# Performance work log

Measured on AMD Instinct MI355X. Metric: run time of the kernel, lower is better.

Reference implementation:

```python
import jax, jax.numpy as jnp
import numpy as np

B, S, D = 2, 2048, 1024
H, DK = 16, 64            # n_heads, d_k = d_model // n_heads
EXP = 4                   # pattern-separation expand_factor
ED = DK * EXP             # expanded_dim = 256
TOPK = 32                 # top-k kept after ReLU expansion
ALPHA = 0.05
TNT = 1.0                 # trace_norm_target


def setup_inputs() -> dict:
    key = jax.random.key(0)
    ks = jax.random.split(key, 8)
    sc = 1.0 / np.sqrt(D)
    x = jax.random.normal(ks[0], (B, S, D), jnp.float32)
    W_q = jax.random.normal(ks[1], (D, D), jnp.float32) * sc
    W_k = jax.random.normal(ks[2], (D, D), jnp.float32) * sc
    W_v = jax.random.normal(ks[3], (D, D), jnp.float32) * sc
    W_o = jax.random.normal(ks[4], (D, D), jnp.float32) * sc
    # trace buffers (non-zero so the trace read path actually matters)
    traces = jax.random.normal(ks[5], (H, DK, DK), jnp.float32) * 0.02
    value_traces = jax.random.normal(ks[6], (H, ED, DK), jnp.float32) * 0.02
    # frozen random expansion projection (dentate gyrus), W / sqrt(d_k)
    W_expand = jax.random.normal(ks[7], (DK, ED), jnp.float32) / np.sqrt(DK)
    return dict(x=x, W_q=W_q, W_k=W_k, W_v=W_v, W_o=W_o,
                traces=traces, value_traces=value_traces, W_expand=W_expand)


def _eff_alpha(T):
    # alpha / (1 + ||T_h||_F / trace_norm_target), shape (1, H, 1, 1)
    norms = jnp.sqrt(jnp.sum(T * T, axis=(1, 2)))
    return (ALPHA / (1.0 + norms / TNT)).reshape(1, -1, 1, 1)


def _forward(x, W_q, W_k, W_v, W_o, traces, value_traces, W_expand):
    b, s, d = x.shape
    def proj(W):
        return jnp.einsum('bsd,de->bse', x, W).reshape(b, s, H, DK).transpose(0, 2, 1, 3)
    Q, K, V = proj(W_q), proj(W_k), proj(W_v)  # (B, H, S, DK)

    scores = jnp.einsum('bhqd,bhkd->bhqk', Q, K)
    # score trace bias: alpha_eff * (Q @ T @ K^T)
    QT = jnp.einsum('bhqd,hde->bhqe', Q, traces)
    trace_scores = jnp.einsum('bhqe,bhke->bhqk', QT, K)
    scores = (scores + _eff_alpha(traces) * trace_scores) / np.sqrt(DK)
    A = jax.nn.softmax(scores, axis=-1)
    out = jnp.einsum('bhqk,bhkd->bhqd', A, V)

    # value trace read with use_key_q shift: address with previous token's Q
    Q_addr = jnp.concatenate([jnp.zeros_like(Q[:, :, :1, :]), Q[:, :, :-1, :]], axis=2)
    # pattern separation: frozen random expansion + ReLU + top-k sparsify
    Q_exp = jax.nn.relu(jnp.einsum('bhsd,de->bhse', Q_addr, W_expand))  # (B,H,S,ED)
    kth = jax.lax.top_k(Q_exp, TOPK)[0][..., -1:]
    Q_sparse = jnp.where(Q_exp >= kth, Q_exp, 0.0)  # == scatter of top-k vals (ties at 0 contribute 0)
    stored = jnp.einsum('bhse,hed->bhsd', Q_sparse, value_traces)
    out = out + _eff_alpha(value_traces) * stored

    out = out.transpose(0, 2, 1, 3).reshape(b, s, d)
    return jnp.einsum('bsd,de->bse', out, W_o)


def reference(x, W_q, W_k, W_v, W_o, traces, value_traces, W_expand):
    return _forward(x, W_q, W_k, W_v, W_o, traces, value_traces, W_expand)
```

## Files before the change

kernel.cpp:

```cpp
#include <hip/hip_runtime.h>
#include <stdint.h>

#define Bn 2
#define Sn 2048
#define Dn 1024
#define Hn 16
#define DKn 64
#define EDn 256

typedef __attribute__((ext_vector_type(8))) short bvec8;
typedef __attribute__((ext_vector_type(4))) float fvec4;

#define MFMA(a, b, c) __builtin_amdgcn_mfma_f32_16x16x32_bf16(a, b, c, 0, 0, 0)

__device__ __forceinline__ float b2f(unsigned short u) {
  return __uint_as_float(((unsigned)u) << 16);
}
__device__ __forceinline__ unsigned short f2b(float x) {
  unsigned u = __float_as_uint(x);
  u += 0x7fffu + ((u >> 16) & 1u);
  return (unsigned short)(u >> 16);
}
__device__ __forceinline__ void g2l(const unsigned short* g, unsigned short* l) {
  __builtin_amdgcn_global_load_lds(
      (const __attribute__((address_space(1))) void*)g,
      (__attribute__((address_space(3))) void*)l, 16, 0, 0);
}

__global__ __launch_bounds__(256) void k_alphas(
    const float* __restrict__ traces, const float* __restrict__ vtr,
    float* __restrict__ alphas) {
  int blk = blockIdx.x;
  const float* base;
  int n;
  if (blk < 16) { base = traces + blk * DKn * DKn; n = DKn * DKn; }
  else          { base = vtr + (blk - 16) * EDn * DKn; n = EDn * DKn; }
  float s = 0.f;
  for (int i = threadIdx.x; i < n; i += 256) { float v = base[i]; s += v * v; }
  __shared__ float red[256];
  red[threadIdx.x] = s;
  __syncthreads();
  for (int off = 128; off > 0; off >>= 1) {
    if (threadIdx.x < off) red[threadIdx.x] += red[threadIdx.x + off];
    __syncthreads();
  }
  if (threadIdx.x == 0) alphas[blk] = 0.05f / (1.f + sqrtf(red[0]));
}

__global__ __launch_bounds__(256) void k_trW(
    const float* __restrict__ w0, const float* __restrict__ w1,
    const float* __restrict__ w2, const float* __restrict__ w3,
    unsigned short* __restrict__ dst) {
  int z = blockIdx.z;
  const float* src = (z == 0) ? w0 : ((z == 1) ? w1 : ((z == 2) ? w2 : w3));
  unsigned short* d = dst + (size_t)z * Dn * Dn;
  __shared__ unsigned short Tl[64][72];
  int tid = threadIdx.x;
  int k0 = blockIdx.y * 64, n0 = blockIdx.x * 64;
#pragma unroll
  for (int i = 0; i < 4; ++i) {
    int q = tid + 256 * i;
    int kr = q >> 4, c4 = q & 15;
    float4 v = *(const float4*)&src[(size_t)(k0 + kr) * Dn + n0 + 4 * c4];
    ushort4 u;
    u.x = f2b(v.x); u.y = f2b(v.y); u.z = f2b(v.z); u.w = f2b(v.w);
    *(ushort4*)&Tl[kr][4 * c4] = u;
  }
  __syncthreads();
#pragma unroll
  for (int i = 0; i < 4; ++i) {
    int q = tid + 256 * i;
    int nr = q >> 4, c4 = q & 15;
    ushort4 u;
    u.x = Tl[4 * c4 + 0][nr]; u.y = Tl[4 * c4 + 1][nr];
    u.z = Tl[4 * c4 + 2][nr]; u.w = Tl[4 * c4 + 3][nr];
    *(ushort4*)&d[(size_t)(n0 + nr) * Dn + k0 + 4 * c4] = u;
  }
}

__global__ __launch_bounds__(256) void k_mkM(const float* __restrict__ tr,
                                             const float* __restrict__ alph,
                                             unsigned short* __restrict__ Mt) {
  int h = blockIdx.x;
  float a = alph[h] * 0.125f;
  const float* th = tr + (size_t)h * DKn * DKn;
  unsigned short* mh = Mt + (size_t)h * DKn * DKn;
  for (int i = threadIdx.x; i < DKn * DKn; i += 256) {
    int e = i >> 6, k = i & 63;
    float v = a * th[(size_t)k * DKn + e] + ((e == k) ? 0.125f : 0.f);
    mh[i] = f2b(v);
  }
}

__global__ __launch_bounds__(256) void k_trE(const float* __restrict__ Wexp,
                                             unsigned short* __restrict__ WexpT) {
  int e0 = blockIdx.x * 64;
  __shared__ unsigned short Tl[64][72];
  int tid = threadIdx.x;
#pragma unroll
  for (int i = 0; i < 4; ++i) {
    int q = tid + 256 * i;
    int dr = q >> 4, c4 = q & 15;
    float4 v = *(const float4*)&Wexp[(size_t)dr * EDn + e0 + 4 * c4];
    ushort4 u;
    u.x = f2b(v.x); u.y = f2b(v.y); u.z = f2b(v.z); u.w = f2b(v.w);
    *(ushort4*)&Tl[dr][4 * c4] = u;
  }
  __syncthreads();
#pragma unroll
  for (int i = 0; i < 4; ++i) {
    int q = tid + 256 * i;
    int er = q >> 4, c4 = q & 15;
    ushort4 u;
    u.x = Tl[4 * c4 + 0][er]; u.y = Tl[4 * c4 + 1][er];
    u.z = Tl[4 * c4 + 2][er]; u.w = Tl[4 * c4 + 3][er];
    *(ushort4*)&WexpT[(size_t)(e0 + er) * DKn + 4 * c4] = u;
  }
}

__global__ __launch_bounds__(256) void k_trVT(const float* __restrict__ vtr,
                                              unsigned short* __restrict__ VTt) {
  int e0 = blockIdx.x * 64;
  int h = blockIdx.y;
  const float* src = vtr + (size_t)h * EDn * DKn;
  unsigned short* dst = VTt + (size_t)h * DKn * EDn;
  __shared__ unsigned short Tl[64][72];
  int tid = threadIdx.x;
#pragma unroll
  for (int i = 0; i < 4; ++i) {
    int q = tid + 256 * i;
    int er = q >> 4, c4 = q & 15;
    float4 v = *(const float4*)&src[(size_t)(e0 + er) * DKn + 4 * c4];
    ushort4 u;
    u.x = f2b(v.x); u.y = f2b(v.y); u.z = f2b(v.z); u.w = f2b(v.w);
    *(ushort4*)&Tl[er][4 * c4] = u;
  }
  __syncthreads();
#pragma unroll
  for (int i = 0; i < 4; ++i) {
    int q = tid + 256 * i;
    int dr = q >> 4, c4 = q & 15;
    ushort4 u;
    u.x = Tl[4 * c4 + 0][dr]; u.y = Tl[4 * c4 + 1][dr];
    u.z = Tl[4 * c4 + 2][dr]; u.w = Tl[4 * c4 + 3][dr];
    *(ushort4*)&dst[(size_t)dr * EDn + e0 + 4 * c4] = u;
  }
}

__global__ __launch_bounds__(256) void k_xb(const float* __restrict__ x,
                                            unsigned short* __restrict__ xb) {
  size_t i = ((size_t)blockIdx.x * 256 + threadIdx.x) * 4;
  float4 v = *(const float4*)&x[i];
  ushort4 u;
  u.x = f2b(v.x); u.y = f2b(v.y); u.z = f2b(v.z); u.w = f2b(v.w);
  *(ushort4*)&xb[i] = u;
}

template <int MODE>
__global__ __launch_bounds__(256) void k_gemm(
    const unsigned short* __restrict__ Ab, const float* __restrict__ Af,
    const unsigned short* __restrict__ BtBase, unsigned short* __restrict__ Qb,
    unsigned short* __restrict__ Kb, unsigned short* __restrict__ VtOut,
    float* __restrict__ Cout) {
  const int z = (MODE == 0) ? blockIdx.z : 0;
  const unsigned short* Bt = BtBase + (size_t)z * Dn * Dn;
  __shared__ unsigned short As[128 * 32];
  __shared__ unsigned short Bs[128 * 32];
  const int tid = threadIdx.x;
  const int w = tid >> 6, lane = tid & 63, qd = lane >> 4, cc = lane & 15;
  const int m0 = blockIdx.y * 128, n0 = blockIdx.x * 128;
  const int mW = 64 * (w >> 1), nW = 64 * (w & 1);
  const int srow = lane >> 2;
  const int schk = 8 * ((lane & 3) ^ (srow & 3));
  const int r0 = 32 * w + srow, r1 = r0 + 16;
  fvec4 acc[4][4];
#pragma unroll
  for (int i = 0; i < 4; ++i)
#pragma unroll
    for (int j = 0; j < 4; ++j) acc[i][j] = (fvec4){0.f, 0.f, 0.f, 0.f};

  for (int k0 = 0; k0 < Dn; k0 += 32) {
    if (MODE == 0) {
      g2l(&Ab[(size_t)(m0 + r0) * Dn + k0 + schk], &As[1024 * w]);
      g2l(&Ab[(size_t)(m0 + r1) * Dn + k0 + schk], &As[1024 * w + 512]);
    } else {
#pragma unroll
      for (int i = 0; i < 4; ++i) {
        int q = tid + 256 * i;
        int row = q >> 3, c4 = q & 7;
        float4 v = *(const float4*)&Af[(size_t)(m0 + row) * Dn + k0 + 4 * c4];
        ushort4 u;
        u.x = f2b(v.x); u.y = f2b(v.y); u.z = f2b(v.z); u.w = f2b(v.w);
        *(ushort4*)&As[row * 32 + 8 * ((c4 >> 1) ^ (row & 3)) + 4 * (c4 & 1)] =
            u;
      }
    }
    g2l(&Bt[(size_t)(n0 + r0) * Dn + k0 + schk], &Bs[1024 * w]);
    g2l(&Bt[(size_t)(n0 + r1) * Dn + k0 + schk], &Bs[1024 * w + 512]);
    __syncthreads();
    bvec8 af[4], bf[4];
#pragma unroll
    for (int i = 0; i < 4; ++i) {
      int ra = mW + 16 * i + cc;
      af[i] = *(const bvec8*)&As[ra * 32 + 8 * (qd ^ (ra & 3))];
      int rb = nW + 16 * i + cc;
      bf[i] = *(const bvec8*)&Bs[rb * 32 + 8 * (qd ^ (rb & 3))];
    }
#pragma unroll
    for (int i = 0; i < 4; ++i)
#pragma unroll
      for (int j = 0; j < 4; ++j) acc[i][j] = MFMA(af[i], bf[j], acc[i][j]);
    __syncthreads();
  }
#pragma unroll
  for (int i = 0; i < 4; ++i)
#pragma unroll
    for (int j = 0; j < 4; ++j) {
      int rowb = m0 + mW + 16 * i + 4 * qd;
      int col = n0 + nW + 16 * j + cc;
      if (MODE == 0) {
        int b = rowb >> 11, s = rowb & 2047;
        int h = col >> 6, dk = col & 63;
        if (z == 2) {
          ushort4 u;
          u.x = f2b(acc[i][j][0]); u.y = f2b(acc[i][j][1]);
          u.z = f2b(acc[i][j][2]); u.w = f2b(acc[i][j][3]);
          *(ushort4*)&VtOut[(((size_t)(b * Hn + h)) * DKn + dk) * Sn + s] = u;
        } else {
          unsigned short* Cb = (z == 0) ? Qb : Kb;
#pragma unroll
          for (int r = 0; r < 4; ++r)
            Cb[(((size_t)(b * Hn + h)) * Sn + s + r) * DKn + dk] =
                f2b(acc[i][j][r]);
        }
      } else {
#pragma unroll
        for (int r = 0; r < 4; ++r)
          Cout[(size_t)(rowb + r) * Dn + col] = acc[i][j][r];
      }
    }
}

__global__ __launch_bounds__(256, 2) void k_pattsep(
    const unsigned short* __restrict__ Qb,
    const unsigned short* __restrict__ WexpT,
    const unsigned short* __restrict__ VTt,
    const float* __restrict__ alphas, float* __restrict__ AT) {
  __shared__ uint4 Wl4[2048];
  __shared__ uint4 Vl4[2048];
  __shared__ uint4 Ps4[4][256];
  const int tile = blockIdx.x, bh = blockIdx.y;
  const int b = bh >> 4, h = bh & 15;
  const int tid = threadIdx.x;
  const int w = tid >> 6, lane = tid & 63, qd = lane >> 4, cc = lane & 15;
  const float avt = alphas[16 + h];

  const uint4* wsrc = (const uint4*)WexpT;
  const uint4* vsrc = (const uint4*)(VTt + (size_t)h * DKn * EDn);
  for (int i = tid; i < 2048; i += 256) {
    int e = i >> 3, c = i & 7;
    Wl4[e * 8 + (c ^ (e & 7))] = wsrc[i];
    int d = i >> 5, c2 = i & 31;
    Vl4[d * 32 + (c2 ^ (d & 7))] = vsrc[i];
  }
  __syncthreads();

  const unsigned short* Wls = (const unsigned short*)Wl4;
  const unsigned short* Vls = (const unsigned short*)Vl4;
  unsigned short* Pw = (unsigned short*)Ps4[w];

  for (int rg = 0; rg < 2; ++rg) {
    const int s0 = tile * 128 + w * 32 + rg * 16;
    bvec8 aq0 = {}, aq1 = {};
    const int srow = s0 + cc;
    if (srow > 0) {
      const unsigned short* qp = Qb + ((size_t)bh * Sn + srow - 1) * DKn;
      aq0 = *(const bvec8*)&qp[8 * qd];
      aq1 = *(const bvec8*)&qp[32 + 8 * qd];
    }
    fvec4 E[16];
#pragma unroll
    for (int j = 0; j < 16; ++j) {
      const int e = 16 * j + cc;
      const unsigned short* wr = Wls + e * 64;
      bvec8 b0 = *(const bvec8*)&wr[8 * (qd ^ (e & 7))];
      bvec8 b1 = *(const bvec8*)&wr[8 * ((4 + qd) ^ (e & 7))];
      fvec4 zv = {0.f, 0.f, 0.f, 0.f};
      zv = MFMA(aq0, b0, zv);
      E[j] = MFMA(aq1, b1, zv);
    }
#pragma unroll
    for (int j = 0; j < 16; ++j)
#pragma unroll
      for (int r = 0; r < 4; ++r) E[j][r] = fmaxf(E[j][r], 0.f);

    float thr[4];
#pragma unroll
    for (int r = 0; r < 4; ++r) {
      unsigned cur = 0u;
      bool done = false;
      for (int bit = 30; bit >= 0; --bit) {
        unsigned cand = cur | (1u << bit);
        float t = __uint_as_float(cand);
        int cnt = 0;
#pragma unroll
        for (int j = 0; j < 16; ++j) cnt += (E[j][r] >= t) ? 1 : 0;
        cnt += __shfl_xor(cnt, 1);
        cnt += __shfl_xor(cnt, 2);
        cnt += __shfl_xor(cnt, 4);
        cnt += __shfl_xor(cnt, 8);
        if (!done && cnt >= 32) {
          cur = cand;
          if (cnt == 32) done = true;
        }
        if (__all(done)) break;
      }
      thr[r] = __uint_as_float(cur);
    }

    fvec4 acc2[4];
#pragma unroll
    for (int j2 = 0; j2 < 4; ++j2) acc2[j2] = (fvec4){0.f, 0.f, 0.f, 0.f};

#pragma unroll
    for (int half = 0; half < 2; ++half) {
#pragma unroll
      for (int j = 0; j < 8; ++j) {
        const int jj = j + 8 * half;
#pragma unroll
        for (int r = 0; r < 4; ++r) {
          float v = E[jj][r];
          bool sel = (v >= thr[r]) && (v > 0.f);
          int row = 4 * qd + r;
          int s = 16 * j + cc;
          int ch = (s >> 3) ^ (row & 7);
          Pw[row * 128 + ch * 8 + (s & 7)] = sel ? f2b(v) : (unsigned short)0;
        }
      }
#pragma unroll
      for (int j2 = 0; j2 < 4; ++j2) {
        const int d = 16 * j2 + cc;
        const unsigned short* vr = Vls + d * 256;
#pragma unroll
        for (int c = 0; c < 4; ++c) {
          int cg = 4 * (c + 4 * half) + qd;
          bvec8 bv = *(const bvec8*)&vr[8 * (cg ^ (d & 7))];
          int ca = 4 * c + qd;
          bvec8 ap = *(const bvec8*)&Pw[cc * 128 + 8 * (ca ^ (cc & 7))];
          acc2[j2] = MFMA(ap, bv, acc2[j2]);
        }
      }
    }
#pragma unroll
    for (int j2 = 0; j2 < 4; ++j2)
#pragma unroll
      for (int r = 0; r < 4; ++r) {
        int row = s0 + 4 * qd + r;
        AT[((size_t)(b * Sn + row)) * Dn + h * DKn + 16 * j2 + cc] =
            avt * acc2[j2][r];
      }
  }
}

__global__ __launch_bounds__(256) void k_attn(
    const unsigned short* __restrict__ Qb, const unsigned short* __restrict__ Kb,
    const unsigned short* __restrict__ Vt, const unsigned short* __restrict__ Mt,
    float* __restrict__ AT) {
  __shared__ unsigned short Kd[64 * 64];
  __shared__ unsigned short Vl[64 * 64];
  __shared__ unsigned short Ps[4][16][72];
  const int bh = blockIdx.x, qt = blockIdx.y;
  const int b = bh >> 4, h = bh & 15;
  const int tid = threadIdx.x;
  const int w = tid >> 6, lane = tid & 63, qd = lane >> 4, cc = lane & 15;
  const float L2E = 1.4426950408889634f;
  const float NB = 23.083120654223414f;

  const unsigned short* qg = Qb + ((size_t)bh * Sn + qt * 64 + w * 16) * DKn;
  bvec8 a0 = *(const bvec8*)&qg[cc * DKn + 8 * qd];
  bvec8 a1 = *(const bvec8*)&qg[cc * DKn + 32 + 8 * qd];
  const unsigned short* mh = Mt + (size_t)h * DKn * DKn;
#pragma unroll
  for (int j = 0; j < 4; ++j) {
    bvec8 b0 = *(const bvec8*)&mh[(size_t)(16 * j + cc) * DKn + 8 * qd];
    bvec8 b1 = *(const bvec8*)&mh[(size_t)(16 * j + cc) * DKn + 32 + 8 * qd];
    fvec4 zz = {0.f, 0.f, 0.f, 0.f};
    zz = MFMA(a0, b0, zz);
    zz = MFMA(a1, b1, zz);
#pragma unroll
    for (int r = 0; r < 4; ++r) {
      int qr = 4 * qd + r;
      Kd[(16 * w + qr) * 64 + 8 * ((2 * j + (cc >> 3)) ^ (qr & 7)) + (cc & 7)] =
          f2b(zz[r]);
    }
  }
  bvec8 aq0 = *(const bvec8*)&Kd[(16 * w + cc) * 64 + 8 * (qd ^ (cc & 7))];
  bvec8 aq1 =
      *(const bvec8*)&Kd[(16 * w + cc) * 64 + 8 * ((qd + 4) ^ (cc & 7))];

  float l_s = 0.f;
  fvec4 O[4];
#pragma unroll
  for (int j = 0; j < 4; ++j) O[j] = (fvec4){0.f, 0.f, 0.f, 0.f};

  const int vrow = lane >> 3;
  const int vchk = 8 * ((lane & 7) ^ (vrow & 7));
  const unsigned short* kgb = Kb + (size_t)bh * Sn * DKn;
  const unsigned short* vgb = Vt + (size_t)bh * DKn * Sn;

  for (int kt = 0; kt < Sn / 64; ++kt) {
    __syncthreads();
    const unsigned short* kg = kgb + (size_t)kt * 64 * DKn;
    g2l(&kg[(size_t)(16 * w + vrow) * 64 + vchk], &Kd[1024 * w]);
    g2l(&kg[(size_t)(16 * w + 8 + vrow) * 64 + vchk], &Kd[1024 * w + 512]);
    g2l(&vgb[(size_t)(16 * w + vrow) * Sn + kt * 64 + vchk], &Vl[1024 * w]);
    g2l(&vgb[(size_t)(16 * w + 8 + vrow) * Sn + kt * 64 + vchk],
        &Vl[1024 * w + 512]);
    __syncthreads();
    fvec4 sc[4];
#pragma unroll
    for (int j = 0; j < 4; ++j) {
      int rk = 16 * j + cc;
      bvec8 b0 = *(const bvec8*)&Kd[rk * 64 + 8 * (qd ^ (cc & 7))];
      bvec8 b1 = *(const bvec8*)&Kd[rk * 64 + 8 * ((qd + 4) ^ (cc & 7))];
      fvec4 zz = {0.f, 0.f, 0.f, 0.f};
      zz = MFMA(b0, aq0, zz);
      sc[j] = MFMA(b1, aq1, zz);
    }
#pragma unroll
    for (int j = 0; j < 4; ++j) {
      float p0 = __builtin_amdgcn_exp2f(fmaf(sc[j][0], L2E, -NB));
      float p1 = __builtin_amdgcn_exp2f(fmaf(sc[j][1], L2E, -NB));
      float p2 = __builtin_amdgcn_exp2f(fmaf(sc[j][2], L2E, -NB));
      float p3 = __builtin_amdgcn_exp2f(fmaf(sc[j][3], L2E, -NB));
      l_s += (p0 + p1) + (p2 + p3);
      ushort4 u;
      u.x = f2b(p0); u.y = f2b(p1); u.z = f2b(p2); u.w = f2b(p3);
      *(ushort4*)&Ps[w][cc][16 * j + 4 * qd] = u;
    }
    bvec8 ap0 = *(const bvec8*)&Ps[w][cc][8 * qd];
    bvec8 ap1 = *(const bvec8*)&Ps[w][cc][32 + 8 * qd];
#pragma unroll
    for (int j = 0; j < 4; ++j) {
      int rv = 16 * j + cc;
      bvec8 v0 = *(const bvec8*)&Vl[rv * 64 + 8 * (qd ^ (cc & 7))];
      bvec8 v1 = *(const bvec8*)&Vl[rv * 64 + 8 * ((qd + 4) ^ (cc & 7))];
      O[j] = MFMA(ap0, v0, O[j]);
      O[j] = MFMA(ap1, v1, O[j]);
    }
  }
  l_s += __shfl_xor(l_s, 16);
  l_s += __shfl_xor(l_s, 32);
  float linv = 1.f / l_s;
  float inv[4];
#pragma unroll
  for (int r = 0; r < 4; ++r) inv[r] = __shfl(linv, 4 * qd + r);
#pragma unroll
  for (int j = 0; j < 4; ++j)
#pragma unroll
    for (int r = 0; r < 4; ++r) {
      int row = qt * 64 + w * 16 + 4 * qd + r;
      float* p = AT + ((size_t)(b * Sn + row)) * Dn + h * DKn + 16 * j + cc;
      *p += O[j][r] * inv[r];
    }
}

extern "C" void kernel_launch(void* const* d_in, const int* in_sizes, int n_in,
                              void* d_out, int out_size, void* d_ws,
                              size_t ws_size, hipStream_t stream) {
  const float* x = (const float*)d_in[0];
  const float* Wq = (const float*)d_in[1];
  const float* Wk = (const float*)d_in[2];
  const float* Wv = (const float*)d_in[3];
  const float* Wo = (const float*)d_in[4];
  const float* traces = (const float*)d_in[5];
  const float* vtr = (const float*)d_in[6];
  const float* Wexp = (const float*)d_in[7];

  const size_t NQ = (size_t)Bn * Hn * Sn * DKn;
  unsigned short* Qb = (unsigned short*)d_ws;
  unsigned short* Kb = Qb + NQ;
  unsigned short* Vt = Kb + NQ;
  unsigned short* Wt = Vt + NQ;
  unsigned short* Mt = Wt + NQ;
  unsigned short* WexpT = Mt + 65536;
  unsigned short* VTt = WexpT + 16384;
  float* alph = (float*)(VTt + 262144);
  float* AT = alph + 32;
  unsigned short* xb = (unsigned short*)AT;

  k_alphas<<<32, 256, 0, stream>>>(traces, vtr, alph);
  k_trW<<<dim3(16, 16, 4), 256, 0, stream>>>(Wq, Wk, Wv, Wo, Wt);
  k_mkM<<<16, 256, 0, stream>>>(traces, alph, Mt);
  k_trE<<<4, 256, 0, stream>>>(Wexp, WexpT);
  k_trVT<<<dim3(4, 16), 256, 0, stream>>>(vtr, VTt);
  k_xb<<<4096, 256, 0, stream>>>(x, xb);
  k_gemm<0><<<dim3(8, 32, 3), 256, 0, stream>>>(xb, nullptr, Wt, Qb, Kb, Vt,
                                                nullptr);
  k_pattsep<<<dim3(16, 32), 256, 0, stream>>>(Qb, WexpT, VTt, alph, AT);
  k_attn<<<dim3(32, 32), 256, 0, stream>>>(Qb, Kb, Vt, Mt, AT);
  k_gemm<1><<<dim3(8, 32, 1), 256, 0, stream>>>(
      nullptr, AT, Wt + 3 * (size_t)Dn * Dn, nullptr, nullptr, nullptr,
      (float*)d_out);
}
```

Before: 309.5 us.

## Merge prep kernels, store attention output in bf16, transpose-free MFMA epilogues

Folds five small preprocessing kernels into one launch, which cuts launch overhead. The attention and pattern-separation output is now stored as bf16, so the final GEMM loads it with global_load_lds instead of converting fp32 per tile, and its buffer traffic is halved. The Q/K and output GEMMs swap the MFMA operands so each lane writes vectorized contiguous stores. The log2e scaling is folded into the M matrix, so softmax drops its fma and max-offset, and a cheaper bf16 pack is used for probabilities. This risks extra rounding in the accumulated output and possible overflow, since the fixed exponent offset is gone.

```diff
diff --git a/kernel.cpp b/kernel.cpp
--- a/kernel.cpp
+++ b/kernel.cpp
@@ -21,144 +21,139 @@
   u += 0x7fffu + ((u >> 16) & 1u);
   return (unsigned short)(u >> 16);
 }
+__device__ __forceinline__ unsigned pk2(float a, float b) {
+  return ((__float_as_uint(a) + 0x8000u) >> 16) |
+         ((__float_as_uint(b) + 0x8000u) & 0xffff0000u);
+}
 __device__ __forceinline__ void g2l(const unsigned short* g, unsigned short* l) {
   __builtin_amdgcn_global_load_lds(
       (const __attribute__((address_space(1))) void*)g,
       (__attribute__((address_space(3))) void*)l, 16, 0, 0);
 }
 
-__global__ __launch_bounds__(256) void k_alphas(
-    const float* __restrict__ traces, const float* __restrict__ vtr,
-    float* __restrict__ alphas) {
-  int blk = blockIdx.x;
-  const float* base;
-  int n;
-  if (blk < 16) { base = traces + blk * DKn * DKn; n = DKn * DKn; }
-  else          { base = vtr + (blk - 16) * EDn * DKn; n = EDn * DKn; }
-  float s = 0.f;
-  for (int i = threadIdx.x; i < n; i += 256) { float v = base[i]; s += v * v; }
-  __shared__ float red[256];
-  red[threadIdx.x] = s;
-  __syncthreads();
-  for (int off = 128; off > 0; off >>= 1) {
-    if (threadIdx.x < off) red[threadIdx.x] += red[threadIdx.x + off];
-    __syncthreads();
-  }
-  if (threadIdx.x == 0) alphas[blk] = 0.05f / (1.f + sqrtf(red[0]));
-}
-
-__global__ __launch_bounds__(256) void k_trW(
-    const float* __restrict__ w0, const float* __restrict__ w1,
-    const float* __restrict__ w2, const float* __restrict__ w3,
-    unsigned short* __restrict__ dst) {
-  int z = blockIdx.z;
-  const float* src = (z == 0) ? w0 : ((z == 1) ? w1 : ((z == 2) ? w2 : w3));
-  unsigned short* d = dst + (size_t)z * Dn * Dn;
+__global__ __launch_bounds__(256) void k_prep1(
+    const float* __restrict__ x, const float* __restrict__ w0,
+    const float* __restrict__ w1, const float* __restrict__ w2,
+    const float* __restrict__ w3, const float* __restrict__ traces,
+    const float* __restrict__ vtr, const float* __restrict__ Wexp,
+    unsigned short* __restrict__ Wt, unsigned short* __restrict__ WexpT,
+    unsigned short* __restrict__ xb, float* __restrict__ alphas,
+    unsigned short* __restrict__ VTt) {
+  const int blk = blockIdx.x;
+  const int tid = threadIdx.x;
   __shared__ unsigned short Tl[64][72];
-  int tid = threadIdx.x;
-  int k0 = blockIdx.y * 64, n0 = blockIdx.x * 64;
-#pragma unroll
-  for (int i = 0; i < 4; ++i) {
-    int q = tid + 256 * i;
-    int kr = q >> 4, c4 = q & 15;
-    float4 v = *(const float4*)&src[(size_t)(k0 + kr) * Dn + n0 + 4 * c4];
+  if (blk < 1024) {
+    int z = blk >> 8, t = blk & 255;
+    int n0 = (t & 15) * 64, k0 = (t >> 4) * 64;
+    const float* src = (z == 0) ? w0 : ((z == 1) ? w1 : ((z == 2) ? w2 : w3));
+    unsigned short* d = Wt + (size_t)z * Dn * Dn;
+#pragma unroll
+    for (int i = 0; i < 4; ++i) {
+      int q = tid + 256 * i;
+      int kr = q >> 4, c4 = q & 15;
+      float4 v = *(const float4*)&src[(size_t)(k0 + kr) * Dn + n0 + 4 * c4];
+      ushort4 u;
+      u.x = f2b(v.x); u.y = f2b(v.y); u.z = f2b(v.z); u.w = f2b(v.w);
+      *(ushort4*)&Tl[kr][4 * c4] = u;
+    }
+    __syncthreads();
+#pragma unroll
+    for (int i = 0; i < 4; ++i) {
+      int q = tid + 256 * i;
+      int nr = q >> 4, c4 = q & 15;
+      ushort4 u;
+      u.x = Tl[4 * c4 + 0][nr]; u.y = Tl[4 * c4 + 1][nr];
+      u.z = Tl[4 * c4 + 2][nr]; u.w = Tl[4 * c4 + 3][nr];
+      *(ushort4*)&d[(size_t)(n0 + nr) * Dn + k0 + 4 * c4] = u;
+    }
+  } else if (blk < 1028) {
+    int e0 = (blk - 1024) * 64;
+#pragma unroll
+    for (int i = 0; i < 4; ++i) {
+      int q = tid + 256 * i;
+      int dr = q >> 4, c4 = q & 15;
+      float4 v = *(const float4*)&Wexp[(size_t)dr * EDn + e0 + 4 * c4];
+      ushort4 u;
+      u.x = f2b(v.x); u.y = f2b(v.y); u.z = f2b(v.z); u.w = f2b(v.w);
+      *(ushort4*)&Tl[dr][4 * c4] = u;
+    }
+    __syncthreads();
+#pragma unroll
+    for (int i = 0; i < 4; ++i) {
+      int q = tid + 256 * i;
+      int er = q >> 4, c4 = q & 15;
+      ushort4 u;
+      u.x = Tl[4 * c4 + 0][er]; u.y = Tl[4 * c4 + 1][er];
+      u.z = Tl[4 * c4 + 2][er]; u.w = Tl[4 * c4 + 3][er];
+      *(ushort4*)&WexpT[(size_t)(e0 + er) * DKn + 4 * c4] = u;
+    }
+  } else if (blk < 5124) {
+    size_t i = ((size_t)(blk - 1028) * 256 + tid) * 4;
+    float4 v = *(const float4*)&x[i];
     ushort4 u;
     u.x = f2b(v.x); u.y = f2b(v.y); u.z = f2b(v.z); u.w = f2b(v.w);
-    *(ushort4*)&Tl[kr][4 * c4] = u;
-  }
-  __syncthreads();
-#pragma unroll
-  for (int i = 0; i < 4; ++i) {
-    int q = tid + 256 * i;
-    int nr = q >> 4, c4 = q & 15;
-    ushort4 u;
-    u.x = Tl[4 * c4 + 0][nr]; u.y = Tl[4 * c4 + 1][nr];
-    u.z = Tl[4 * c4 + 2][nr]; u.w = Tl[4 * c4 + 3][nr];
-    *(ushort4*)&d[(size_t)(n0 + nr) * Dn + k0 + 4 * c4] = u;
+    *(ushort4*)&xb[i] = u;
+  } else if (blk < 5156) {
+    int a = blk - 5124;
+    const float* base;
+    int n;
+    if (a < 16) { base = traces + a * DKn * DKn; n = DKn * DKn; }
+    else        { base = vtr + (a - 16) * EDn * DKn; n = EDn * DKn; }
+    float s = 0.f;
+    for (int i = tid; i < n; i += 256) { float v = base[i]; s += v * v; }
+    __shared__ float red[256];
+    red[tid] = s;
+    __syncthreads();
+    for (int off = 128; off > 0; off >>= 1) {
+      if (tid < off) red[tid] += red[tid + off];
+      __syncthreads();
+    }
+    if (tid == 0) alphas[a] = 0.05f / (1.f + sqrtf(red[0]));
+  } else {
+    int t = blk - 5156;
+    int e0 = (t & 3) * 64, h = t >> 2;
+    const float* src = vtr + (size_t)h * EDn * DKn;
+    unsigned short* dst = VTt + (size_t)h * DKn * EDn;
+#pragma unroll
+    for (int i = 0; i < 4; ++i) {
+      int q = tid + 256 * i;
+      int er = q >> 4, c4 = q & 15;
+      float4 v = *(const float4*)&src[(size_t)(e0 + er) * DKn + 4 * c4];
+      ushort4 u;
+      u.x = f2b(v.x); u.y = f2b(v.y); u.z = f2b(v.z); u.w = f2b(v.w);
+      *(ushort4*)&Tl[er][4 * c4] = u;
+    }
+    __syncthreads();
+#pragma unroll
+    for (int i = 0; i < 4; ++i) {
+      int q = tid + 256 * i;
+      int dr = q >> 4, c4 = q & 15;
+      ushort4 u;
+      u.x = Tl[4 * c4 + 0][dr]; u.y = Tl[4 * c4 + 1][dr];
+      u.z = Tl[4 * c4 + 2][dr]; u.w = Tl[4 * c4 + 3][dr];
+      *(ushort4*)&dst[(size_t)dr * EDn + e0 + 4 * c4] = u;
+    }
   }
 }
 
 __global__ __launch_bounds__(256) void k_mkM(const float* __restrict__ tr,
                                              const float* __restrict__ alph,
                                              unsigned short* __restrict__ Mt) {
+  const float SC = 0.125f * 1.4426950408889634f;
   int h = blockIdx.x;
-  float a = alph[h] * 0.125f;
+  float a = alph[h] * SC;
   const float* th = tr + (size_t)h * DKn * DKn;
   unsigned short* mh = Mt + (size_t)h * DKn * DKn;
   for (int i = threadIdx.x; i < DKn * DKn; i += 256) {
     int e = i >> 6, k = i & 63;
-    float v = a * th[(size_t)k * DKn + e] + ((e == k) ? 0.125f : 0.f);
+    float v = a * th[(size_t)k * DKn + e] + ((e == k) ? SC : 0.f);
     mh[i] = f2b(v);
   }
-}
-
-__global__ __launch_bounds__(256) void k_trE(const float* __restrict__ Wexp,
-                                             unsigned short* __restrict__ WexpT) {
-  int e0 = blockIdx.x * 64;
-  __shared__ unsigned short Tl[64][72];
-  int tid = threadIdx.x;
-#pragma unroll
-  for (int i = 0; i < 4; ++i) {
-    int q = tid + 256 * i;
-    int dr = q >> 4, c4 = q & 15;
-    float4 v = *(const float4*)&Wexp[(size_t)dr * EDn + e0 + 4 * c4];
-    ushort4 u;
-    u.x = f2b(v.x); u.y = f2b(v.y); u.z = f2b(v.z); u.w = f2b(v.w);
-    *(ushort4*)&Tl[dr][4 * c4] = u;
-  }
-  __syncthreads();
-#pragma unroll
-  for (int i = 0; i < 4; ++i) {
-    int q = tid + 256 * i;
-    int er = q >> 4, c4 = q & 15;
-    ushort4 u;
-    u.x = Tl[4 * c4 + 0][er]; u.y = Tl[4 * c4 + 1][er];
-    u.z = Tl[4 * c4 + 2][er]; u.w = Tl[4 * c4 + 3][er];
-    *(ushort4*)&WexpT[(size_t)(e0 + er) * DKn + 4 * c4] = u;
-  }
-}
-
-__global__ __launch_bounds__(256) void k_trVT(const float* __restrict__ vtr,
-                                              unsigned short* __restrict__ VTt) {
-  int e0 = blockIdx.x * 64;
-  int h = blockIdx.y;
-  const float* src = vtr + (size_t)h * EDn * DKn;
-  unsigned short* dst = VTt + (size_t)h * DKn * EDn;
-  __shared__ unsigned short Tl[64][72];
-  int tid = threadIdx.x;
-#pragma unroll
-  for (int i = 0; i < 4; ++i) {
-    int q = tid + 256 * i;
-    int er = q >> 4, c4 = q & 15;
-    float4 v = *(const float4*)&src[(size_t)(e0 + er) * DKn + 4 * c4];
-    ushort4 u;
-    u.x = f2b(v.x); u.y = f2b(v.y); u.z = f2b(v.z); u.w = f2b(v.w);
-    *(ushort4*)&Tl[er][4 * c4] = u;
-  }
-  __syncthreads();
-#pragma unroll
-  for (int i = 0; i < 4; ++i) {
-    int q = tid + 256 * i;
-    int dr = q >> 4, c4 = q & 15;
-    ushort4 u;
-    u.x = Tl[4 * c4 + 0][dr]; u.y = Tl[4 * c4 + 1][dr];
-    u.z = Tl[4 * c4 + 2][dr]; u.w = Tl[4 * c4 + 3][dr];
-    *(ushort4*)&dst[(size_t)dr * EDn + e0 + 4 * c4] = u;
-  }
-}
-
-__global__ __launch_bounds__(256) void k_xb(const float* __restrict__ x,
-                                            unsigned short* __restrict__ xb) {
-  size_t i = ((size_t)blockIdx.x * 256 + threadIdx.x) * 4;
-  float4 v = *(const float4*)&x[i];
-  ushort4 u;
-  u.x = f2b(v.x); u.y = f2b(v.y); u.z = f2b(v.z); u.w = f2b(v.w);
-  *(ushort4*)&xb[i] = u;
 }
 
 template <int MODE>
 __global__ __launch_bounds__(256) void k_gemm(
-    const unsigned short* __restrict__ Ab, const float* __restrict__ Af,
+    const unsigned short* __restrict__ Ab,
     const unsigned short* __restrict__ BtBase, unsigned short* __restrict__ Qb,
     unsigned short* __restrict__ Kb, unsigned short* __restrict__ VtOut,
     float* __restrict__ Cout) {
@@ -173,6 +168,7 @@
   const int srow = lane >> 2;
   const int schk = 8 * ((lane & 3) ^ (srow & 3));
   const int r0 = 32 * w + srow, r1 = r0 + 16;
+  const bool swap = (MODE == 1) || (z != 2);
   fvec4 acc[4][4];
 #pragma unroll
   for (int i = 0; i < 4; ++i)
@@ -180,21 +176,8 @@
     for (int j = 0; j < 4; ++j) acc[i][j] = (fvec4){0.f, 0.f, 0.f, 0.f};
 
   for (int k0 = 0; k0 < Dn; k0 += 32) {
-    if (MODE == 0) {
-      g2l(&Ab[(size_t)(m0 + r0) * Dn + k0 + schk], &As[1024 * w]);
-      g2l(&Ab[(size_t)(m0 + r1) * Dn + k0 + schk], &As[1024 * w + 512]);
-    } else {
-#pragma unroll
-      for (int i = 0; i < 4; ++i) {
-        int q = tid + 256 * i;
-        int row = q >> 3, c4 = q & 7;
-        float4 v = *(const float4*)&Af[(size_t)(m0 + row) * Dn + k0 + 4 * c4];
-        ushort4 u;
-        u.x = f2b(v.x); u.y = f2b(v.y); u.z = f2b(v.z); u.w = f2b(v.w);
-        *(ushort4*)&As[row * 32 + 8 * ((c4 >> 1) ^ (row & 3)) + 4 * (c4 & 1)] =
-            u;
-      }
-    }
+    g2l(&Ab[(size_t)(m0 + r0) * Dn + k0 + schk], &As[1024 * w]);
+    g2l(&Ab[(size_t)(m0 + r1) * Dn + k0 + schk], &As[1024 * w + 512]);
     g2l(&Bt[(size_t)(n0 + r0) * Dn + k0 + schk], &Bs[1024 * w]);
     g2l(&Bt[(size_t)(n0 + r1) * Dn + k0 + schk], &Bs[1024 * w + 512]);
     __syncthreads();
@@ -206,37 +189,49 @@
       int rb = nW + 16 * i + cc;
       bf[i] = *(const bvec8*)&Bs[rb * 32 + 8 * (qd ^ (rb & 3))];
     }
-#pragma unroll
-    for (int i = 0; i < 4; ++i)
-#pragma unroll
-      for (int j = 0; j < 4; ++j) acc[i][j] = MFMA(af[i], bf[j], acc[i][j]);
+    if (swap) {
+#pragma unroll
+      for (int i = 0; i < 4; ++i)
+#pragma unroll
+        for (int j = 0; j < 4; ++j) acc[i][j] = MFMA(bf[j], af[i], acc[i][j]);
+    } else {
+#pragma unroll
+      for (int i = 0; i < 4; ++i)
+#pragma unroll
+        for (int j = 0; j < 4; ++j) acc[i][j] = MFMA(af[i], bf[j], acc[i][j]);
+    }
     __syncthreads();
   }
 #pragma unroll
   for (int i = 0; i < 4; ++i)
 #pragma unroll
     for (int j = 0; j < 4; ++j) {
-      int rowb = m0 + mW + 16 * i + 4 * qd;
-      int col = n0 + nW + 16 * j + cc;
-      if (MODE == 0) {
+      if (MODE == 1) {
+        int s = m0 + mW + 16 * i + cc;
+        int nb = n0 + nW + 16 * j + 4 * qd;
+        float4 v = make_float4(acc[i][j][0], acc[i][j][1], acc[i][j][2],
+                               acc[i][j][3]);
+        *(float4*)&Cout[(size_t)s * Dn + nb] = v;
+      } else if (z == 2) {
+        int rowb = m0 + mW + 16 * i + 4 * qd;
+        int col = n0 + nW + 16 * j + cc;
         int b = rowb >> 11, s = rowb & 2047;
         int h = col >> 6, dk = col & 63;
-        if (z == 2) {
-          ushort4 u;
-          u.x = f2b(acc[i][j][0]); u.y = f2b(acc[i][j][1]);
-          u.z = f2b(acc[i][j][2]); u.w = f2b(acc[i][j][3]);
-          *(ushort4*)&VtOut[(((size_t)(b * Hn + h)) * DKn + dk) * Sn + s] = u;
-        } else {
-          unsigned short* Cb = (z == 0) ? Qb : Kb;
-#pragma unroll
-          for (int r = 0; r < 4; ++r)
-            Cb[(((size_t)(b * Hn + h)) * Sn + s + r) * DKn + dk] =
-                f2b(acc[i][j][r]);
-        }
+        ushort4 u;
+        u.x = f2b(acc[i][j][0]); u.y = f2b(acc[i][j][1]);
+        u.z = f2b(acc[i][j][2]); u.w = f2b(acc[i][j][3]);
+        *(ushort4*)&VtOut[(((size_t)(b * Hn + h)) * DKn + dk) * Sn + s] = u;
       } else {
-#pragma unroll
-        for (int r = 0; r < 4; ++r)
-          Cout[(size_t)(rowb + r) * Dn + col] = acc[i][j][r];
+        int s = m0 + mW + 16 * i + cc;
+        int col = n0 + nW + 16 * j + 4 * qd;
+        int b = s >> 11;
+        int sm = s & 2047;
+        int h = col >> 6, dk = col & 63;
+        unsigned short* Cb = (z == 0) ? Qb : Kb;
+        ushort4 u;
+        u.x = f2b(acc[i][j][0]); u.y = f2b(acc[i][j][1]);
+        u.z = f2b(acc[i][j][2]); u.w = f2b(acc[i][j][3]);
+        *(ushort4*)&Cb[(((size_t)(b * Hn + h)) * Sn + sm) * DKn + dk] = u;
       }
     }
 }
@@ -245,7 +240,7 @@
     const unsigned short* __restrict__ Qb,
     const unsigned short* __restrict__ WexpT,
     const unsigned short* __restrict__ VTt,
-    const float* __restrict__ alphas, float* __restrict__ AT) {
+    const float* __restrict__ alphas, unsigned short* __restrict__ ATb) {
   __shared__ uint4 Wl4[2048];
   __shared__ uint4 Vl4[2048];
   __shared__ uint4 Ps4[4][256];
@@ -356,8 +351,8 @@
 #pragma unroll
       for (int r = 0; r < 4; ++r) {
         int row = s0 + 4 * qd + r;
-        AT[((size_t)(b * Sn + row)) * Dn + h * DKn + 16 * j2 + cc] =
-            avt * acc2[j2][r];
+        ATb[((size_t)(b * Sn + row)) * Dn + h * DKn + 16 * j2 + cc] =
+            f2b(avt * acc2[j2][r]);
       }
   }
 }
@@ -365,7 +360,7 @@
 __global__ __launch_bounds__(256) void k_attn(
     const unsigned short* __restrict__ Qb, const unsigned short* __restrict__ Kb,
     const unsigned short* __restrict__ Vt, const unsigned short* __restrict__ Mt,
-    float* __restrict__ AT) {
+    unsigned short* __restrict__ ATb) {
   __shared__ unsigned short Kd[64 * 64];
   __shared__ unsigned short Vl[64 * 64];
   __shared__ unsigned short Ps[4][16][72];
@@ -373,8 +368,6 @@
   const int b = bh >> 4, h = bh & 15;
   const int tid = threadIdx.x;
   const int w = tid >> 6, lane = tid & 63, qd = lane >> 4, cc = lane & 15;
-  const float L2E = 1.4426950408889634f;
-  const float NB = 23.083120654223414f;
 
   const unsigned short* qg = Qb + ((size_t)bh * Sn + qt * 64 + w * 16) * DKn;
   bvec8 a0 = *(const bvec8*)&qg[cc * DKn + 8 * qd];
@@ -429,14 +422,15 @@
     }
 #pragma unroll
     for (int j = 0; j < 4; ++j) {
-      float p0 = __builtin_amdgcn_exp2f(fmaf(sc[j][0], L2E, -NB));
-      float p1 = __builtin_amdgcn_exp2f(fmaf(sc[j][1], L2E, -NB));
-      float p2 = __builtin_amdgcn_exp2f(fmaf(sc[j][2], L2E, -NB));
-      float p3 = __builtin_amdgcn_exp2f(fmaf(sc[j][3], L2E, -NB));
+      float p0 = __builtin_amdgcn_exp2f(sc[j][0]);
+      float p1 = __builtin_amdgcn_exp2f(sc[j][1]);
+      float p2 = __builtin_amdgcn_exp2f(sc[j][2]);
+      float p3 = __builtin_amdgcn_exp2f(sc[j][3]);
       l_s += (p0 + p1) + (p2 + p3);
-      ushort4 u;
-      u.x = f2b(p0); u.y = f2b(p1); u.z = f2b(p2); u.w = f2b(p3);
-      *(ushort4*)&Ps[w][cc][16 * j + 4 * qd] = u;
+      uint2 u;
+      u.x = pk2(p0, p1);
+      u.y = pk2(p2, p3);
+      *(uint2*)&Ps[w][cc][16 * j + 4 * qd] = u;
     }
     bvec8 ap0 = *(const bvec8*)&Ps[w][cc][8 * qd];
     bvec8 ap1 = *(const bvec8*)&Ps[w][cc][32 + 8 * qd];
@@ -460,8 +454,9 @@
 #pragma unroll
     for (int r = 0; r < 4; ++r) {
       int row = qt * 64 + w * 16 + 4 * qd + r;
-      float* p = AT + ((size_t)(b * Sn + row)) * Dn + h * DKn + 16 * j + cc;
-      *p += O[j][r] * inv[r];
+      unsigned short* p =
+          ATb + ((size_t)(b * Sn + row)) * Dn + h * DKn + 16 * j + cc;
+      *p = f2b(b2f(*p) + O[j][r] * inv[r]);
     }
 }
 
@@ -486,20 +481,16 @@
   unsigned short* WexpT = Mt + 65536;
   unsigned short* VTt = WexpT + 16384;
   float* alph = (float*)(VTt + 262144);
-  float* AT = alph + 32;
-  unsigned short* xb = (unsigned short*)AT;
-
-  k_alphas<<<32, 256, 0, stream>>>(traces, vtr, alph);
-  k_trW<<<dim3(16, 16, 4), 256, 0, stream>>>(Wq, Wk, Wv, Wo, Wt);
+  unsigned short* ATb = (unsigned short*)(alph + 32);
+  unsigned short* xb = ATb;
+
+  k_prep1<<<5220, 256, 0, stream>>>(x, Wq, Wk, Wv, Wo, traces, vtr, Wexp, Wt,
+                                    WexpT, xb, alph, VTt);
   k_mkM<<<16, 256, 0, stream>>>(traces, alph, Mt);
-  k_trE<<<4, 256, 0, stream>>>(Wexp, WexpT);
-  k_trVT<<<dim3(4, 16), 256, 0, stream>>>(vtr, VTt);
-  k_xb<<<4096, 256, 0, stream>>>(x, xb);
-  k_gemm<0><<<dim3(8, 32, 3), 256, 0, stream>>>(xb, nullptr, Wt, Qb, Kb, Vt,
-                                                nullptr);
-  k_pattsep<<<dim3(16, 32), 256, 0, stream>>>(Qb, WexpT, VTt, alph, AT);
-  k_attn<<<dim3(32, 32), 256, 0, stream>>>(Qb, Kb, Vt, Mt, AT);
+  k_gemm<0><<<dim3(8, 32, 3), 256, 0, stream>>>(xb, Wt, Qb, Kb, Vt, nullptr);
+  k_pattsep<<<dim3(16, 32), 256, 0, stream>>>(Qb, WexpT, VTt, alph, ATb);
+  k_attn<<<dim3(32, 32), 256, 0, stream>>>(Qb, Kb, Vt, Mt, ATb);
   k_gemm<1><<<dim3(8, 32, 1), 256, 0, stream>>>(
-      nullptr, AT, Wt + 3 * (size_t)Dn * Dn, nullptr, nullptr, nullptr,
+      ATb, Wt + 3 * (size_t)Dn * Dn, nullptr, nullptr, nullptr,
       (float*)d_out);
 }
```

After: 315.4 us. About the same (+1.9%).
